# Optimization experiments

Measured on AMD Instinct MI355X. Metric: run time of the kernel, lower is better.

Reference implementation:

```python
import jax, jax.numpy as jnp
import numpy as np

HIDDEN = 1024
INTER = 4096
EPS = 1e-12


def _ste(q, x):
    # straight-through estimator: forward q, backward identity wrt x
    return x + jax.lax.stop_gradient(q - x)


def setup_inputs() -> dict:
    key = jax.random.key(0)
    ks = jax.random.split(key, 4)
    hidden_states = jax.random.normal(ks[0], (4, 2048, INTER), dtype=jnp.float32)
    input_tensor = jax.random.normal(ks[1], (4, 2048, HIDDEN), dtype=jnp.float32)
    W = jax.random.normal(ks[2], (HIDDEN, INTER), dtype=jnp.float32) * 0.02
    b = jnp.zeros((HIDDEN,), dtype=jnp.float32)
    clip_val = jnp.asarray(2.5, dtype=jnp.float32)  # learnable elastic alpha
    gamma = jnp.ones((HIDDEN,), dtype=jnp.float32)
    beta = jnp.zeros((HIDDEN,), dtype=jnp.float32)
    return {"hidden_states": hidden_states, "input_tensor": input_tensor,
            "W": W, "b": b, "clip_val": clip_val, "gamma": gamma, "beta": beta}


def reference(hidden_states, input_tensor, W, b, clip_val, gamma, beta):
    # --- binary weight (BWN): per-output-channel scale = mean(|W|, axis=in) ---
    w_scale = jnp.mean(jnp.abs(W), axis=1, keepdims=True)  # [hidden, 1]
    W_q = _ste(w_scale * jnp.sign(W), W)                    # [hidden, inter]
    # --- elastic signed binary activation: q = alpha * sign(x / alpha) ---
    s = hidden_states / clip_val
    x_q = clip_val * _ste(jnp.sign(s), s)                   # [b, s, inter]
    # --- dense projection ---
    h = jnp.einsum('bsi,hi->bsh', x_q, W_q) + b             # [b, s, hidden]
    # dropout prob 0.0 (eval mode) -> no-op
    # --- residual + LayerNorm (eps=1e-12) ---
    r = h + input_tensor
    mu = jnp.mean(r, axis=-1, keepdims=True)
    var = jnp.mean(jnp.square(r - mu), axis=-1, keepdims=True)
    out = (r - mu) * jax.lax.rsqrt(var + EPS) * gamma + beta
    return out
```

## Files before the change

kernel.cpp:

```cpp
#include <hip/hip_runtime.h>
#include <stdint.h>

#define HIDDEN 1024
#define INTER  4096
#define NWORDS 64
#define ROWS   8192
#define MT     8
#define GBLK   (ROWS / MT)

typedef unsigned long long u64;

__global__ __launch_bounds__(256)
void pack_kernel(const float* __restrict__ hs, const float* __restrict__ W,
                 u64* __restrict__ abits_t, u64* __restrict__ wbits_t,
                 float* __restrict__ wscale) {
    int lane = threadIdx.x & 63;
    int wave = threadIdx.x >> 6;
    int b = blockIdx.x;

    if (b < ROWS / 4) {
        int m = b * 4 + wave;
        const float* row = hs + (size_t)m * INTER;
        u64* dst = abits_t + (size_t)(m >> 3) * NWORDS * MT + (m & 7);
        #pragma unroll 4
        for (int w = 0; w < NWORDS; ++w) {
            float x = row[w * 64 + lane];
            u64 mask = __ballot(x < 0.0f);
            if (lane == 0) dst[(size_t)w * MT] = mask;
        }
    } else {
        int h = b - ROWS / 4;
        const float* row = W + (size_t)h * INTER;
        float asum = 0.f;
        for (int w = wave; w < NWORDS; w += 4) {
            float x = row[w * 64 + lane];
            asum += fabsf(x);
            u64 mask = __ballot(x < 0.0f);
            if (lane == 0) wbits_t[(size_t)w * HIDDEN + h] = mask;
        }
        #pragma unroll
        for (int off = 32; off > 0; off >>= 1) asum += __shfl_down(asum, off);
        __shared__ float red[4];
        if (lane == 0) red[wave] = asum;
        __syncthreads();
        if (threadIdx.x == 0)
            wscale[h] = (red[0] + red[1] + red[2] + red[3]) * (1.0f / INTER);
    }
}

__global__ __launch_bounds__(256, 4)
void gemm_ln_kernel(const u64* __restrict__ abits_t, const u64* __restrict__ wbits_t,
                    const float* __restrict__ wscale, const float* __restrict__ bias,
                    const float* __restrict__ clipp, const float* __restrict__ input,
                    const float* __restrict__ gamma, const float* __restrict__ beta,
                    float* __restrict__ out) {
    int t  = threadIdx.x;
    int m0 = blockIdx.x * MT;
    int h0 = t * 4;
    const u64* ablk = abits_t + (size_t)blockIdx.x * NWORDS * MT;

    int acc[MT][4];
    #pragma unroll
    for (int mi = 0; mi < MT; ++mi)
        #pragma unroll
        for (int c = 0; c < 4; ++c) acc[mi][c] = 0;

    #pragma unroll 2
    for (int k = 0; k < NWORDS; ++k) {
        const u64* wp = wbits_t + (size_t)k * HIDDEN + h0;
        u64 w0 = wp[0];
        u64 w1 = wp[1];
        u64 w2 = wp[2];
        u64 w3 = wp[3];
        const u64* ap = ablk + k * MT;
        #pragma unroll
        for (int mi = 0; mi < MT; ++mi) {
            u64 a = ap[mi];
            acc[mi][0] += __popcll(a ^ w0);
            acc[mi][1] += __popcll(a ^ w1);
            acc[mi][2] += __popcll(a ^ w2);
            acc[mi][3] += __popcll(a ^ w3);
        }
    }

    float clip = clipp[0];
    float4 cw = reinterpret_cast<const float4*>(wscale)[t];
    cw.x *= clip; cw.y *= clip; cw.z *= clip; cw.w *= clip;
    float4 bi = reinterpret_cast<const float4*>(bias)[t];
    float4 gm = reinterpret_cast<const float4*>(gamma)[t];
    float4 bt = reinterpret_cast<const float4*>(beta)[t];

    float vals[MT][4];
    #pragma unroll
    for (int mi = 0; mi < MT; ++mi) {
        float4 inp = reinterpret_cast<const float4*>(input + (size_t)(m0 + mi) * HIDDEN)[t];
        vals[mi][0] = fmaf((float)(INTER - 2 * acc[mi][0]), cw.x, bi.x + inp.x);
        vals[mi][1] = fmaf((float)(INTER - 2 * acc[mi][1]), cw.y, bi.y + inp.y);
        vals[mi][2] = fmaf((float)(INTER - 2 * acc[mi][2]), cw.z, bi.z + inp.z);
        vals[mi][3] = fmaf((float)(INTER - 2 * acc[mi][3]), cw.w, bi.w + inp.w);
    }

    __shared__ float red_s[4][MT];
    __shared__ float red_q[4][MT];
    __shared__ float s_mu[MT], s_rs[MT];
    int lane = t & 63, wave = t >> 6;
    #pragma unroll
    for (int mi = 0; mi < MT; ++mi) {
        float s = vals[mi][0] + vals[mi][1] + vals[mi][2] + vals[mi][3];
        float q = vals[mi][0] * vals[mi][0] + vals[mi][1] * vals[mi][1]
                + vals[mi][2] * vals[mi][2] + vals[mi][3] * vals[mi][3];
        #pragma unroll
        for (int off = 32; off > 0; off >>= 1) {
            s += __shfl_down(s, off);
            q += __shfl_down(q, off);
        }
        if (lane == 0) { red_s[wave][mi] = s; red_q[wave][mi] = q; }
    }
    __syncthreads();
    if (t < MT) {
        float s = red_s[0][t] + red_s[1][t] + red_s[2][t] + red_s[3][t];
        float q = red_q[0][t] + red_q[1][t] + red_q[2][t] + red_q[3][t];
        float mu  = s * (1.0f / HIDDEN);
        float var = fmaf(-mu, mu, q * (1.0f / HIDDEN));
        s_mu[t] = mu;
        s_rs[t] = rsqrtf(var + 1e-12f);
    }
    __syncthreads();

    #pragma unroll
    for (int mi = 0; mi < MT; ++mi) {
        float mu = s_mu[mi], rs = s_rs[mi];
        float4 o;
        o.x = (vals[mi][0] - mu) * rs * gm.x + bt.x;
        o.y = (vals[mi][1] - mu) * rs * gm.y + bt.y;
        o.z = (vals[mi][2] - mu) * rs * gm.z + bt.z;
        o.w = (vals[mi][3] - mu) * rs * gm.w + bt.w;
        reinterpret_cast<float4*>(out + (size_t)(m0 + mi) * HIDDEN)[t] = o;
    }
}

extern "C" void kernel_launch(void* const* d_in, const int* in_sizes, int n_in,
                              void* d_out, int out_size, void* d_ws, size_t ws_size,
                              hipStream_t stream) {
    const float* hs    = (const float*)d_in[0];
    const float* inp   = (const float*)d_in[1];
    const float* W     = (const float*)d_in[2];
    const float* b     = (const float*)d_in[3];
    const float* clip  = (const float*)d_in[4];
    const float* gamma = (const float*)d_in[5];
    const float* beta  = (const float*)d_in[6];
    float* out = (float*)d_out;

    u64*   abits  = (u64*)d_ws;
    u64*   wbits  = (u64*)((char*)d_ws + (size_t)ROWS * NWORDS * 8);
    float* wscale = (float*)((char*)d_ws + (size_t)ROWS * NWORDS * 8
                                         + (size_t)NWORDS * HIDDEN * 8);

    pack_kernel<<<ROWS / 4 + HIDDEN, 256, 0, stream>>>(hs, W, abits, wbits, wscale);
    gemm_ln_kernel<<<GBLK, 256, 0, stream>>>(abits, wbits, wscale, b, clip,
                                             inp, gamma, beta, out);
}
```

Measured before the change: 333.7 us.

## Fuse activation sign-packing into the GEMM+LayerNorm kernel via shared memory

```diff
diff --git a/kernel.cpp b/kernel.cpp
--- a/kernel.cpp
+++ b/kernel.cpp
@@ -4,61 +4,82 @@
 #define HIDDEN 1024
 #define INTER  4096
 #define NWORDS 64
+#define NCHUNK 16
 #define ROWS   8192
 #define MT     8
 #define GBLK   (ROWS / MT)
 
 typedef unsigned long long u64;
 
+
 __global__ __launch_bounds__(256)
-void pack_kernel(const float* __restrict__ hs, const float* __restrict__ W,
-                 u64* __restrict__ abits_t, u64* __restrict__ wbits_t,
-                 float* __restrict__ wscale) {
+void pack_w_kernel(const float* __restrict__ W, u64* __restrict__ wbits_t,
+                   float* __restrict__ wscale) {
+    int h    = blockIdx.x;
     int lane = threadIdx.x & 63;
     int wave = threadIdx.x >> 6;
-    int b = blockIdx.x;
-
-    if (b < ROWS / 4) {
-        int m = b * 4 + wave;
-        const float* row = hs + (size_t)m * INTER;
-        u64* dst = abits_t + (size_t)(m >> 3) * NWORDS * MT + (m & 7);
-        #pragma unroll 4
-        for (int w = 0; w < NWORDS; ++w) {
-            float x = row[w * 64 + lane];
-            u64 mask = __ballot(x < 0.0f);
-            if (lane == 0) dst[(size_t)w * MT] = mask;
+    const float4* row = (const float4*)(W + (size_t)h * INTER);
+    float asum = 0.f;
+    #pragma unroll
+    for (int c = wave; c < NCHUNK; c += 4) {
+        float4 v = row[c * 64 + lane];
+        asum += fabsf(v.x) + fabsf(v.y) + fabsf(v.z) + fabsf(v.w);
+        u64 b0 = __ballot(v.x < 0.0f);
+        u64 b1 = __ballot(v.y < 0.0f);
+        u64 b2 = __ballot(v.z < 0.0f);
+        u64 b3 = __ballot(v.w < 0.0f);
+        if (lane == 0) {
+            u64* dst = wbits_t + (size_t)(4 * c) * HIDDEN + h;
+            dst[0 * HIDDEN] = b0;
+            dst[1 * HIDDEN] = b1;
+            dst[2 * HIDDEN] = b2;
+            dst[3 * HIDDEN] = b3;
         }
-    } else {
-        int h = b - ROWS / 4;
-        const float* row = W + (size_t)h * INTER;
-        float asum = 0.f;
-        for (int w = wave; w < NWORDS; w += 4) {
-            float x = row[w * 64 + lane];
-            asum += fabsf(x);
-            u64 mask = __ballot(x < 0.0f);
-            if (lane == 0) wbits_t[(size_t)w * HIDDEN + h] = mask;
-        }
-        #pragma unroll
-        for (int off = 32; off > 0; off >>= 1) asum += __shfl_down(asum, off);
-        __shared__ float red[4];
-        if (lane == 0) red[wave] = asum;
-        __syncthreads();
-        if (threadIdx.x == 0)
-            wscale[h] = (red[0] + red[1] + red[2] + red[3]) * (1.0f / INTER);
     }
+    #pragma unroll
+    for (int off = 32; off > 0; off >>= 1) asum += __shfl_down(asum, off);
+    __shared__ float red[4];
+    if (lane == 0) red[wave] = asum;
+    __syncthreads();
+    if (threadIdx.x == 0)
+        wscale[h] = (red[0] + red[1] + red[2] + red[3]) * (1.0f / INTER);
 }
 
 __global__ __launch_bounds__(256, 4)
-void gemm_ln_kernel(const u64* __restrict__ abits_t, const u64* __restrict__ wbits_t,
-                    const float* __restrict__ wscale, const float* __restrict__ bias,
-                    const float* __restrict__ clipp, const float* __restrict__ input,
-                    const float* __restrict__ gamma, const float* __restrict__ beta,
-                    float* __restrict__ out) {
-    int t  = threadIdx.x;
-    int m0 = blockIdx.x * MT;
+void main_kernel(const float* __restrict__ hs, const u64* __restrict__ wbits_t,
+                 const float* __restrict__ wscale, const float* __restrict__ bias,
+                 const float* __restrict__ clipp, const float* __restrict__ input,
+                 const float* __restrict__ gamma, const float* __restrict__ beta,
+                 float* __restrict__ out) {
+    int t    = threadIdx.x;
+    int lane = t & 63;
+    int wave = t >> 6;
+    int m0   = blockIdx.x * MT;
+
+    __shared__ u64 sA[MT][NWORDS];
+
+    #pragma unroll
+    for (int r = 0; r < 2; ++r) {
+        int mi = wave * 2 + r;
+        const float4* row = (const float4*)(hs + (size_t)(m0 + mi) * INTER);
+        #pragma unroll
+        for (int c = 0; c < NCHUNK; ++c) {
+            float4 v = row[c * 64 + lane];
+            u64 b0 = __ballot(v.x < 0.0f);
+            u64 b1 = __ballot(v.y < 0.0f);
+            u64 b2 = __ballot(v.z < 0.0f);
+            u64 b3 = __ballot(v.w < 0.0f);
+            if (lane == 0) {
+                sA[mi][4 * c + 0] = b0;
+                sA[mi][4 * c + 1] = b1;
+                sA[mi][4 * c + 2] = b2;
+                sA[mi][4 * c + 3] = b3;
+            }
+        }
+    }
+    __syncthreads();
+
     int h0 = t * 4;
-    const u64* ablk = abits_t + (size_t)blockIdx.x * NWORDS * MT;
-
     int acc[MT][4];
     #pragma unroll
     for (int mi = 0; mi < MT; ++mi)
@@ -68,18 +89,19 @@
     #pragma unroll 2
     for (int k = 0; k < NWORDS; ++k) {
         const u64* wp = wbits_t + (size_t)k * HIDDEN + h0;
-        u64 w0 = wp[0];
-        u64 w1 = wp[1];
-        u64 w2 = wp[2];
-        u64 w3 = wp[3];
-        const u64* ap = ablk + k * MT;
+        ulonglong2 wA = ((const ulonglong2*)wp)[0];
+        ulonglong2 wB = ((const ulonglong2*)wp)[1];
         #pragma unroll
         for (int mi = 0; mi < MT; ++mi) {
-            u64 a = ap[mi];
-            acc[mi][0] += __popcll(a ^ w0);
-            acc[mi][1] += __popcll(a ^ w1);
-            acc[mi][2] += __popcll(a ^ w2);
-            acc[mi][3] += __popcll(a ^ w3);
+            u64 a  = sA[mi][k];
+            u64 x0 = a ^ wA.x;
+            u64 x1 = a ^ wA.y;
+            u64 x2 = a ^ wB.x;
+            u64 x3 = a ^ wB.y;
+            acc[mi][0] += __popc((uint32_t)x0) + __popc((uint32_t)(x0 >> 32));
+            acc[mi][1] += __popc((uint32_t)x1) + __popc((uint32_t)(x1 >> 32));
+            acc[mi][2] += __popc((uint32_t)x2) + __popc((uint32_t)(x2 >> 32));
+            acc[mi][3] += __popc((uint32_t)x3) + __popc((uint32_t)(x3 >> 32));
         }
     }
 
@@ -103,7 +125,6 @@
     __shared__ float red_s[4][MT];
     __shared__ float red_q[4][MT];
     __shared__ float s_mu[MT], s_rs[MT];
-    int lane = t & 63, wave = t >> 6;
     #pragma unroll
     for (int mi = 0; mi < MT; ++mi) {
         float s = vals[mi][0] + vals[mi][1] + vals[mi][2] + vals[mi][3];
@@ -151,12 +172,10 @@
     const float* beta  = (const float*)d_in[6];
     float* out = (float*)d_out;
 
-    u64*   abits  = (u64*)d_ws;
-    u64*   wbits  = (u64*)((char*)d_ws + (size_t)ROWS * NWORDS * 8);
-    float* wscale = (float*)((char*)d_ws + (size_t)ROWS * NWORDS * 8
-                                         + (size_t)NWORDS * HIDDEN * 8);
+    u64*   wbits  = (u64*)d_ws;
+    float* wscale = (float*)((char*)d_ws + (size_t)NWORDS * HIDDEN * 8);
 
-    pack_kernel<<<ROWS / 4 + HIDDEN, 256, 0, stream>>>(hs, W, abits, wbits, wscale);
-    gemm_ln_kernel<<<GBLK, 256, 0, stream>>>(abits, wbits, wscale, b, clip,
-                                             inp, gamma, beta, out);
+    pack_w_kernel<<<HIDDEN, 256, 0, stream>>>(W, wbits, wscale);
+    main_kernel<<<GBLK, 256, 0, stream>>>(hs, wbits, wscale, b, clip,
+                                          inp, gamma, beta, out);
 }
```

Result: faster. 312.1 us (-6.5%).

## Vectorize sign packing with float4 ballots and widen binary GEMM block to 512 threads

Applied to the files above, without the earlier changes.

```diff
diff --git a/kernel.cpp b/kernel.cpp
--- a/kernel.cpp
+++ b/kernel.cpp
@@ -7,119 +7,128 @@
 #define ROWS   8192
 #define MT     8
 #define GBLK   (ROWS / MT)
+#define GTHR   512
 
 typedef unsigned long long u64;
 
+
 __global__ __launch_bounds__(256)
 void pack_kernel(const float* __restrict__ hs, const float* __restrict__ W,
-                 u64* __restrict__ abits_t, u64* __restrict__ wbits_t,
+                 u64* __restrict__ abits, u64* __restrict__ wbits,
                  float* __restrict__ wscale) {
     int lane = threadIdx.x & 63;
-    int wave = threadIdx.x >> 6;
-    int b = blockIdx.x;
+    int wv   = threadIdx.x >> 6;
+    int gw   = blockIdx.x * 4 + wv;
+    int l4   = lane & 3;
+    int lc   = lane >> 2;
 
-    if (b < ROWS / 4) {
-        int m = b * 4 + wave;
-        const float* row = hs + (size_t)m * INTER;
-        u64* dst = abits_t + (size_t)(m >> 3) * NWORDS * MT + (m & 7);
-        #pragma unroll 4
-        for (int w = 0; w < NWORDS; ++w) {
-            float x = row[w * 64 + lane];
-            u64 mask = __ballot(x < 0.0f);
-            if (lane == 0) dst[(size_t)w * MT] = mask;
+    if (gw < ROWS) {
+        const float4* row = (const float4*)(hs + (size_t)gw * INTER);
+        u64 myword = 0;
+        #pragma unroll
+        for (int c = 0; c < 16; ++c) {
+            float4 v = row[c * 64 + lane];
+            u64 b0 = __ballot(v.x < 0.0f);
+            u64 b1 = __ballot(v.y < 0.0f);
+            u64 b2 = __ballot(v.z < 0.0f);
+            u64 b3 = __ballot(v.w < 0.0f);
+            u64 sel = b0;
+            sel = (l4 == 1) ? b1 : sel;
+            sel = (l4 == 2) ? b2 : sel;
+            sel = (l4 == 3) ? b3 : sel;
+            myword = (lc == c) ? sel : myword;
         }
+        abits[(size_t)(gw >> 3) * NWORDS * MT + (size_t)lane * MT + (gw & 7)] = myword;
     } else {
-        int h = b - ROWS / 4;
-        const float* row = W + (size_t)h * INTER;
+        int h = gw - ROWS;
+        const float4* row = (const float4*)(W + (size_t)h * INTER);
+        u64 myword = 0;
         float asum = 0.f;
-        for (int w = wave; w < NWORDS; w += 4) {
-            float x = row[w * 64 + lane];
-            asum += fabsf(x);
-            u64 mask = __ballot(x < 0.0f);
-            if (lane == 0) wbits_t[(size_t)w * HIDDEN + h] = mask;
+        #pragma unroll
+        for (int c = 0; c < 16; ++c) {
+            float4 v = row[c * 64 + lane];
+            asum += fabsf(v.x) + fabsf(v.y) + fabsf(v.z) + fabsf(v.w);
+            u64 b0 = __ballot(v.x < 0.0f);
+            u64 b1 = __ballot(v.y < 0.0f);
+            u64 b2 = __ballot(v.z < 0.0f);
+            u64 b3 = __ballot(v.w < 0.0f);
+            u64 sel = b0;
+            sel = (l4 == 1) ? b1 : sel;
+            sel = (l4 == 2) ? b2 : sel;
+            sel = (l4 == 3) ? b3 : sel;
+            myword = (lc == c) ? sel : myword;
         }
+        wbits[(size_t)lane * HIDDEN + h] = myword;
         #pragma unroll
         for (int off = 32; off > 0; off >>= 1) asum += __shfl_down(asum, off);
-        __shared__ float red[4];
-        if (lane == 0) red[wave] = asum;
-        __syncthreads();
-        if (threadIdx.x == 0)
-            wscale[h] = (red[0] + red[1] + red[2] + red[3]) * (1.0f / INTER);
+        if (lane == 0) wscale[h] = asum * (1.0f / INTER);
     }
 }
 
-__global__ __launch_bounds__(256, 4)
-void gemm_ln_kernel(const u64* __restrict__ abits_t, const u64* __restrict__ wbits_t,
+__global__ __launch_bounds__(GTHR, 8)
+void gemm_ln_kernel(const u64* __restrict__ abits, const u64* __restrict__ wbits,
                     const float* __restrict__ wscale, const float* __restrict__ bias,
                     const float* __restrict__ clipp, const float* __restrict__ input,
                     const float* __restrict__ gamma, const float* __restrict__ beta,
                     float* __restrict__ out) {
     int t  = threadIdx.x;
     int m0 = blockIdx.x * MT;
-    int h0 = t * 4;
-    const u64* ablk = abits_t + (size_t)blockIdx.x * NWORDS * MT;
+    int h0 = t * 2;
+    const u64* ablk = abits + (size_t)blockIdx.x * NWORDS * MT;
 
-    int acc[MT][4];
+    int acc[MT][2];
     #pragma unroll
-    for (int mi = 0; mi < MT; ++mi)
-        #pragma unroll
-        for (int c = 0; c < 4; ++c) acc[mi][c] = 0;
+    for (int mi = 0; mi < MT; ++mi) { acc[mi][0] = 0; acc[mi][1] = 0; }
 
-    #pragma unroll 2
+    #pragma unroll 4
     for (int k = 0; k < NWORDS; ++k) {
-        const u64* wp = wbits_t + (size_t)k * HIDDEN + h0;
-        u64 w0 = wp[0];
-        u64 w1 = wp[1];
-        u64 w2 = wp[2];
-        u64 w3 = wp[3];
+        ulonglong2 w = *(const ulonglong2*)(wbits + (size_t)k * HIDDEN + h0);
         const u64* ap = ablk + k * MT;
         #pragma unroll
         for (int mi = 0; mi < MT; ++mi) {
-            u64 a = ap[mi];
-            acc[mi][0] += __popcll(a ^ w0);
-            acc[mi][1] += __popcll(a ^ w1);
-            acc[mi][2] += __popcll(a ^ w2);
-            acc[mi][3] += __popcll(a ^ w3);
+            u64 a  = ap[mi];
+            u64 x0 = a ^ w.x;
+            u64 x1 = a ^ w.y;
+            acc[mi][0] += __popc((uint32_t)x0) + __popc((uint32_t)(x0 >> 32));
+            acc[mi][1] += __popc((uint32_t)x1) + __popc((uint32_t)(x1 >> 32));
         }
     }
 
     float clip = clipp[0];
-    float4 cw = reinterpret_cast<const float4*>(wscale)[t];
-    cw.x *= clip; cw.y *= clip; cw.z *= clip; cw.w *= clip;
-    float4 bi = reinterpret_cast<const float4*>(bias)[t];
-    float4 gm = reinterpret_cast<const float4*>(gamma)[t];
-    float4 bt = reinterpret_cast<const float4*>(beta)[t];
+    float2 cw = reinterpret_cast<const float2*>(wscale)[t];
+    cw.x *= clip; cw.y *= clip;
+    float2 bi = reinterpret_cast<const float2*>(bias)[t];
+    float2 gm = reinterpret_cast<const float2*>(gamma)[t];
+    float2 bt = reinterpret_cast<const float2*>(beta)[t];
 
-    float vals[MT][4];
+    float vals[MT][2];
     #pragma unroll
     for (int mi = 0; mi < MT; ++mi) {
-        float4 inp = reinterpret_cast<const float4*>(input + (size_t)(m0 + mi) * HIDDEN)[t];
+        float2 inp = reinterpret_cast<const float2*>(input + (size_t)(m0 + mi) * HIDDEN)[t];
         vals[mi][0] = fmaf((float)(INTER - 2 * acc[mi][0]), cw.x, bi.x + inp.x);
         vals[mi][1] = fmaf((float)(INTER - 2 * acc[mi][1]), cw.y, bi.y + inp.y);
-        vals[mi][2] = fmaf((float)(INTER - 2 * acc[mi][2]), cw.z, bi.z + inp.z);
-        vals[mi][3] = fmaf((float)(INTER - 2 * acc[mi][3]), cw.w, bi.w + inp.w);
     }
 
-    __shared__ float red_s[4][MT];
-    __shared__ float red_q[4][MT];
+    __shared__ float red_s[8][MT];
+    __shared__ float red_q[8][MT];
     __shared__ float s_mu[MT], s_rs[MT];
-    int lane = t & 63, wave = t >> 6;
+    int lane = t & 63, wv = t >> 6;
     #pragma unroll
     for (int mi = 0; mi < MT; ++mi) {
-        float s = vals[mi][0] + vals[mi][1] + vals[mi][2] + vals[mi][3];
-        float q = vals[mi][0] * vals[mi][0] + vals[mi][1] * vals[mi][1]
-                + vals[mi][2] * vals[mi][2] + vals[mi][3] * vals[mi][3];
+        float s = vals[mi][0] + vals[mi][1];
+        float q = vals[mi][0] * vals[mi][0] + vals[mi][1] * vals[mi][1];
         #pragma unroll
         for (int off = 32; off > 0; off >>= 1) {
             s += __shfl_down(s, off);
             q += __shfl_down(q, off);
         }
-        if (lane == 0) { red_s[wave][mi] = s; red_q[wave][mi] = q; }
+        if (lane == 0) { red_s[wv][mi] = s; red_q[wv][mi] = q; }
     }
     __syncthreads();
     if (t < MT) {
-        float s = red_s[0][t] + red_s[1][t] + red_s[2][t] + red_s[3][t];
-        float q = red_q[0][t] + red_q[1][t] + red_q[2][t] + red_q[3][t];
+        float s = 0.f, q = 0.f;
+        #pragma unroll
+        for (int w = 0; w < 8; ++w) { s += red_s[w][t]; q += red_q[w][t]; }
         float mu  = s * (1.0f / HIDDEN);
         float var = fmaf(-mu, mu, q * (1.0f / HIDDEN));
         s_mu[t] = mu;
@@ -130,12 +139,10 @@
     #pragma unroll
     for (int mi = 0; mi < MT; ++mi) {
         float mu = s_mu[mi], rs = s_rs[mi];
-        float4 o;
+        float2 o;
         o.x = (vals[mi][0] - mu) * rs * gm.x + bt.x;
         o.y = (vals[mi][1] - mu) * rs * gm.y + bt.y;
-        o.z = (vals[mi][2] - mu) * rs * gm.z + bt.z;
-        o.w = (vals[mi][3] - mu) * rs * gm.w + bt.w;
-        reinterpret_cast<float4*>(out + (size_t)(m0 + mi) * HIDDEN)[t] = o;
+        reinterpret_cast<float2*>(out + (size_t)(m0 + mi) * HIDDEN)[t] = o;
     }
 }
 
@@ -156,7 +163,7 @@
     float* wscale = (float*)((char*)d_ws + (size_t)ROWS * NWORDS * 8
                                          + (size_t)NWORDS * HIDDEN * 8);
 
-    pack_kernel<<<ROWS / 4 + HIDDEN, 256, 0, stream>>>(hs, W, abits, wbits, wscale);
-    gemm_ln_kernel<<<GBLK, 256, 0, stream>>>(abits, wbits, wscale, b, clip,
-                                             inp, gamma, beta, out);
+    pack_kernel<<<(ROWS + HIDDEN) / 4, 256, 0, stream>>>(hs, W, abits, wbits, wscale);
+    gemm_ln_kernel<<<GBLK, GTHR, 0, stream>>>(abits, wbits, wscale, b, clip,
+                                              inp, gamma, beta, out);
 }
```

After: 319.2 us. 4.3% less time.

## Replace XOR-popcount GEMM with int8 MFMA on sign-expanded operands

Applied to the files above, without the earlier changes.

```diff
diff --git a/kernel.cpp b/kernel.cpp
--- a/kernel.cpp
+++ b/kernel.cpp
@@ -3,123 +3,180 @@
 
 #define HIDDEN 1024
 #define INTER  4096
-#define NWORDS 64
 #define ROWS   8192
-#define MT     8
-#define GBLK   (ROWS / MT)
+#define BM     32
+#define GTHR   1024
+#define KSUP   512
+#define NSUP   (INTER / KSUP)
 
 typedef unsigned long long u64;
+typedef int v4i __attribute__((ext_vector_type(4)));
+
+__device__ __forceinline__ unsigned sbyte(float x) { return x < 0.0f ? 0xFFu : 0x01u; }
 
 __global__ __launch_bounds__(256)
 void pack_kernel(const float* __restrict__ hs, const float* __restrict__ W,
-                 u64* __restrict__ abits_t, u64* __restrict__ wbits_t,
+                 u64* __restrict__ abits, unsigned char* __restrict__ w8,
                  float* __restrict__ wscale) {
     int lane = threadIdx.x & 63;
     int wave = threadIdx.x >> 6;
     int b = blockIdx.x;
 
-    if (b < ROWS / 4) {
-        int m = b * 4 + wave;
-        const float* row = hs + (size_t)m * INTER;
-        u64* dst = abits_t + (size_t)(m >> 3) * NWORDS * MT + (m & 7);
-        #pragma unroll 4
-        for (int w = 0; w < NWORDS; ++w) {
+    if (b < ROWS) {
+        const float* row = hs + (size_t)b * INTER;
+        u64* dst = abits + (size_t)b * 64;
+        #pragma unroll
+        for (int w = wave; w < 64; w += 4) {
             float x = row[w * 64 + lane];
-            u64 mask = __ballot(x < 0.0f);
-            if (lane == 0) dst[(size_t)w * MT] = mask;
+            u64 m = __ballot(x < 0.0f);
+            if (lane == 0) dst[w] = m;
         }
     } else {
-        int h = b - ROWS / 4;
-        const float* row = W + (size_t)h * INTER;
-        float asum = 0.f;
-        for (int w = wave; w < NWORDS; w += 4) {
-            float x = row[w * 64 + lane];
-            asum += fabsf(x);
-            u64 mask = __ballot(x < 0.0f);
-            if (lane == 0) wbits_t[(size_t)w * HIDDEN + h] = mask;
-        }
+        int h = b - ROWS;
+        int t = threadIdx.x;
+        const float4* row4 = (const float4*)(W + (size_t)h * INTER);
+        float4 v0 = row4[t * 4 + 0];
+        float4 v1 = row4[t * 4 + 1];
+        float4 v2 = row4[t * 4 + 2];
+        float4 v3 = row4[t * 4 + 3];
+        float asum = fabsf(v0.x) + fabsf(v0.y) + fabsf(v0.z) + fabsf(v0.w)
+                   + fabsf(v1.x) + fabsf(v1.y) + fabsf(v1.z) + fabsf(v1.w)
+                   + fabsf(v2.x) + fabsf(v2.y) + fabsf(v2.z) + fabsf(v2.w)
+                   + fabsf(v3.x) + fabsf(v3.y) + fabsf(v3.z) + fabsf(v3.w);
+        uint4 ub;
+        ub.x = sbyte(v0.x) | (sbyte(v0.y) << 8) | (sbyte(v0.z) << 16) | (sbyte(v0.w) << 24);
+        ub.y = sbyte(v1.x) | (sbyte(v1.y) << 8) | (sbyte(v1.z) << 16) | (sbyte(v1.w) << 24);
+        ub.z = sbyte(v2.x) | (sbyte(v2.y) << 8) | (sbyte(v2.z) << 16) | (sbyte(v2.w) << 24);
+        ub.w = sbyte(v3.x) | (sbyte(v3.y) << 8) | (sbyte(v3.z) << 16) | (sbyte(v3.w) << 24);
+        ((uint4*)(w8 + (size_t)h * INTER))[t] = ub;
+
         #pragma unroll
         for (int off = 32; off > 0; off >>= 1) asum += __shfl_down(asum, off);
         __shared__ float red[4];
         if (lane == 0) red[wave] = asum;
         __syncthreads();
-        if (threadIdx.x == 0)
-            wscale[h] = (red[0] + red[1] + red[2] + red[3]) * (1.0f / INTER);
-    }
-}
-
-__global__ __launch_bounds__(256, 4)
-void gemm_ln_kernel(const u64* __restrict__ abits_t, const u64* __restrict__ wbits_t,
+        if (t == 0) wscale[h] = (red[0] + red[1] + red[2] + red[3]) * (1.0f / INTER);
+    }
+}
+
+__device__ __forceinline__ unsigned expand4(unsigned bits) {
+    unsigned spread = (bits & 1u) | ((bits & 2u) << 7) | ((bits & 4u) << 14) | ((bits & 8u) << 21);
+    return 0x01010101u + spread * 0xFEu;
+}
+
+__global__ __launch_bounds__(GTHR, 4)
+void gemm_ln_kernel(const u64* __restrict__ abits, const unsigned char* __restrict__ w8,
                     const float* __restrict__ wscale, const float* __restrict__ bias,
                     const float* __restrict__ clipp, const float* __restrict__ input,
                     const float* __restrict__ gamma, const float* __restrict__ beta,
                     float* __restrict__ out) {
-    int t  = threadIdx.x;
-    int m0 = blockIdx.x * MT;
-    int h0 = t * 4;
-    const u64* ablk = abits_t + (size_t)blockIdx.x * NWORDS * MT;
-
-    int acc[MT][4];
-    #pragma unroll
-    for (int mi = 0; mi < MT; ++mi)
-        #pragma unroll
-        for (int c = 0; c < 4; ++c) acc[mi][c] = 0;
-
-    #pragma unroll 2
-    for (int k = 0; k < NWORDS; ++k) {
-        const u64* wp = wbits_t + (size_t)k * HIDDEN + h0;
-        u64 w0 = wp[0];
-        u64 w1 = wp[1];
-        u64 w2 = wp[2];
-        u64 w3 = wp[3];
-        const u64* ap = ablk + k * MT;
-        #pragma unroll
-        for (int mi = 0; mi < MT; ++mi) {
-            u64 a = ap[mi];
-            acc[mi][0] += __popcll(a ^ w0);
-            acc[mi][1] += __popcll(a ^ w1);
-            acc[mi][2] += __popcll(a ^ w2);
-            acc[mi][3] += __popcll(a ^ w3);
-        }
+    __shared__ uint4 sA[2][GTHR];
+    __shared__ float red_s[BM][17];
+    __shared__ float red_q[BM][17];
+    __shared__ float s_mu[BM], s_rs[BM];
+
+    int t = threadIdx.x;
+    int lane = t & 63, wave = t >> 6, quad = lane >> 4, l15 = lane & 15;
+    int m0 = blockIdx.x * BM;
+    int wbase = wave * 64;
+
+    int ksj  = t >> 7;
+    int rem  = t & 127;
+    int mtj  = rem >> 6;
+    int lj   = rem & 63;
+    int rowj = mtj * 16 + (lj & 15);
+    int koffj = ksj * 64 + (lj >> 4) * 16;
+    const u64* arow = abits + (size_t)(m0 + rowj) * 64;
+    int wordoff = koffj >> 6;
+    int shift   = ((koffj >> 4) & 3) * 16;
+
+    v4i acc[2][4];
+    #pragma unroll
+    for (int mt = 0; mt < 2; ++mt)
+        #pragma unroll
+        for (int nt = 0; nt < 4; ++nt) acc[mt][nt] = (v4i){0, 0, 0, 0};
+
+    auto fetch = [&](int s) -> uint4 {
+        u64 a = arow[s * 8 + wordoff];
+        unsigned hh = (unsigned)(a >> shift) & 0xFFFFu;
+        uint4 r;
+        r.x = expand4(hh);
+        r.y = expand4(hh >> 4);
+        r.z = expand4(hh >> 8);
+        r.w = expand4(hh >> 12);
+        return r;
+    };
+
+    sA[0][t] = fetch(0);
+    __syncthreads();
+
+    for (int s = 0; s < NSUP; ++s) {
+        if (s + 1 < NSUP) sA[(s + 1) & 1][t] = fetch(s + 1);
+        const uint4* buf = sA[s & 1];
+        int kg = s * KSUP;
+        #pragma unroll
+        for (int ks = 0; ks < KSUP / 64; ++ks) {
+            v4i aF0 = *(const v4i*)&buf[(ks * 2 + 0) * 64 + lane];
+            v4i aF1 = *(const v4i*)&buf[(ks * 2 + 1) * 64 + lane];
+            #pragma unroll
+            for (int nt = 0; nt < 4; ++nt) {
+                int n = wbase + nt * 16 + l15;
+                v4i bF = *(const v4i*)(w8 + (size_t)n * INTER + kg + ks * 64 + quad * 16);
+                acc[0][nt] = __builtin_amdgcn_mfma_i32_16x16x64_i8(aF0, bF, acc[0][nt], 0, 0, 0);
+                acc[1][nt] = __builtin_amdgcn_mfma_i32_16x16x64_i8(aF1, bF, acc[1][nt], 0, 0, 0);
+            }
+        }
+        __syncthreads();
     }
 
     float clip = clipp[0];
-    float4 cw = reinterpret_cast<const float4*>(wscale)[t];
-    cw.x *= clip; cw.y *= clip; cw.z *= clip; cw.w *= clip;
-    float4 bi = reinterpret_cast<const float4*>(bias)[t];
-    float4 gm = reinterpret_cast<const float4*>(gamma)[t];
-    float4 bt = reinterpret_cast<const float4*>(beta)[t];
-
-    float vals[MT][4];
-    #pragma unroll
-    for (int mi = 0; mi < MT; ++mi) {
-        float4 inp = reinterpret_cast<const float4*>(input + (size_t)(m0 + mi) * HIDDEN)[t];
-        vals[mi][0] = fmaf((float)(INTER - 2 * acc[mi][0]), cw.x, bi.x + inp.x);
-        vals[mi][1] = fmaf((float)(INTER - 2 * acc[mi][1]), cw.y, bi.y + inp.y);
-        vals[mi][2] = fmaf((float)(INTER - 2 * acc[mi][2]), cw.z, bi.z + inp.z);
-        vals[mi][3] = fmaf((float)(INTER - 2 * acc[mi][3]), cw.w, bi.w + inp.w);
-    }
-
-    __shared__ float red_s[4][MT];
-    __shared__ float red_q[4][MT];
-    __shared__ float s_mu[MT], s_rs[MT];
-    int lane = t & 63, wave = t >> 6;
-    #pragma unroll
-    for (int mi = 0; mi < MT; ++mi) {
-        float s = vals[mi][0] + vals[mi][1] + vals[mi][2] + vals[mi][3];
-        float q = vals[mi][0] * vals[mi][0] + vals[mi][1] * vals[mi][1]
-                + vals[mi][2] * vals[mi][2] + vals[mi][3] * vals[mi][3];
-        #pragma unroll
-        for (int off = 32; off > 0; off >>= 1) {
-            s += __shfl_down(s, off);
-            q += __shfl_down(q, off);
-        }
-        if (lane == 0) { red_s[wave][mi] = s; red_q[wave][mi] = q; }
-    }
+    float cw[4], bi[4], gm[4], bt[4];
+    #pragma unroll
+    for (int nt = 0; nt < 4; ++nt) {
+        int n = wbase + nt * 16 + l15;
+        cw[nt] = clip * wscale[n];
+        bi[nt] = bias[n];
+        gm[nt] = gamma[n];
+        bt[nt] = beta[n];
+    }
+
+    float vals[2][4][4];
+    #pragma unroll
+    for (int mt = 0; mt < 2; ++mt)
+        #pragma unroll
+        for (int reg = 0; reg < 4; ++reg) {
+            int m = m0 + mt * 16 + quad * 4 + reg;
+            const float* irow = input + (size_t)m * HIDDEN;
+            #pragma unroll
+            for (int nt = 0; nt < 4; ++nt) {
+                int n = wbase + nt * 16 + l15;
+                vals[mt][nt][reg] = fmaf((float)acc[mt][nt][reg], cw[nt], bi[nt] + irow[n]);
+            }
+        }
+
+    #pragma unroll
+    for (int mt = 0; mt < 2; ++mt)
+        #pragma unroll
+        for (int reg = 0; reg < 4; ++reg) {
+            float s = vals[mt][0][reg] + vals[mt][1][reg] + vals[mt][2][reg] + vals[mt][3][reg];
+            float q = vals[mt][0][reg] * vals[mt][0][reg] + vals[mt][1][reg] * vals[mt][1][reg]
+                    + vals[mt][2][reg] * vals[mt][2][reg] + vals[mt][3][reg] * vals[mt][3][reg];
+            #pragma unroll
+            for (int off = 1; off < 16; off <<= 1) {
+                s += __shfl_xor(s, off);
+                q += __shfl_xor(q, off);
+            }
+            if (l15 == 0) {
+                int r = mt * 16 + quad * 4 + reg;
+                red_s[r][wave] = s;
+                red_q[r][wave] = q;
+            }
+        }
     __syncthreads();
-    if (t < MT) {
-        float s = red_s[0][t] + red_s[1][t] + red_s[2][t] + red_s[3][t];
-        float q = red_q[0][t] + red_q[1][t] + red_q[2][t] + red_q[3][t];
+    if (t < BM) {
+        float s = 0.f, q = 0.f;
+        #pragma unroll
+        for (int w = 0; w < 16; ++w) { s += red_s[t][w]; q += red_q[t][w]; }
         float mu  = s * (1.0f / HIDDEN);
         float var = fmaf(-mu, mu, q * (1.0f / HIDDEN));
         s_mu[t] = mu;
@@ -128,15 +185,18 @@
     __syncthreads();
 
     #pragma unroll
-    for (int mi = 0; mi < MT; ++mi) {
-        float mu = s_mu[mi], rs = s_rs[mi];
-        float4 o;
-        o.x = (vals[mi][0] - mu) * rs * gm.x + bt.x;
-        o.y = (vals[mi][1] - mu) * rs * gm.y + bt.y;
-        o.z = (vals[mi][2] - mu) * rs * gm.z + bt.z;
-        o.w = (vals[mi][3] - mu) * rs * gm.w + bt.w;
-        reinterpret_cast<float4*>(out + (size_t)(m0 + mi) * HIDDEN)[t] = o;
-    }
+    for (int mt = 0; mt < 2; ++mt)
+        #pragma unroll
+        for (int reg = 0; reg < 4; ++reg) {
+            int r = mt * 16 + quad * 4 + reg;
+            float mu = s_mu[r], rs = s_rs[r];
+            float* orow = out + (size_t)(m0 + r) * HIDDEN;
+            #pragma unroll
+            for (int nt = 0; nt < 4; ++nt) {
+                int n = wbase + nt * 16 + l15;
+                orow[n] = (vals[mt][nt][reg] - mu) * rs * gm[nt] + bt[nt];
+            }
+        }
 }
 
 extern "C" void kernel_launch(void* const* d_in, const int* in_sizes, int n_in,
@@ -151,12 +211,13 @@
     const float* beta  = (const float*)d_in[6];
     float* out = (float*)d_out;
 
-    u64*   abits  = (u64*)d_ws;
-    u64*   wbits  = (u64*)((char*)d_ws + (size_t)ROWS * NWORDS * 8);
-    float* wscale = (float*)((char*)d_ws + (size_t)ROWS * NWORDS * 8
-                                         + (size_t)NWORDS * HIDDEN * 8);
-
-    pack_kernel<<<ROWS / 4 + HIDDEN, 256, 0, stream>>>(hs, W, abits, wbits, wscale);
-    gemm_ln_kernel<<<GBLK, 256, 0, stream>>>(abits, wbits, wscale, b, clip,
-                                             inp, gamma, beta, out);
-}
+    u64*           abits  = (u64*)d_ws;
+    unsigned char* w8     = (unsigned char*)d_ws + (size_t)ROWS * 64 * 8;
+    float*         wscale = (float*)((unsigned char*)d_ws
+                                     + (size_t)ROWS * 64 * 8
+                                     + (size_t)HIDDEN * INTER);
+
+    pack_kernel<<<ROWS + HIDDEN, 256, 0, stream>>>(hs, W, abits, w8, wscale);
+    gemm_ln_kernel<<<ROWS / BM, GTHR, 0, stream>>>(abits, w8, wscale, b, clip,
+                                                   inp, gamma, beta, out);
+}
```

Result: slower. 374.8 us (+12.3%).
